# Kernel optimization log

Measured on AMD Instinct MI355X. Metric: run time of the kernel, lower is better.

Reference implementation:

```python
import jax, jax.numpy as jnp
import numpy as np

N_NODES = 50000
N_RAND_EDGES = 800000
K_HEADS = 4
D = 64
EPS = 1e-8


def setup_inputs() -> dict:
    key = jax.random.key(0)
    k1, k2, k3, k4, k5, k6 = jax.random.split(key, 6)
    x = jax.random.normal(k1, (N_NODES, D), dtype=jnp.float32)
    # edge_index without self loops (module removes then re-adds them), then append self loops
    dst = jax.random.randint(k2, (N_RAND_EDGES,), 0, N_NODES)
    off = jax.random.randint(k3, (N_RAND_EDGES,), 1, N_NODES)
    src = (dst + off) % N_NODES  # guaranteed src != dst
    loops = jnp.arange(N_NODES)
    adj = jnp.stack([jnp.concatenate([dst, loops]), jnp.concatenate([src, loops])]).astype(jnp.int64)
    e = jax.random.uniform(k4, (N_NODES, K_HEADS), dtype=jnp.float32)
    stdv = 1.0 / np.sqrt(D)
    weights = jax.random.uniform(k5, (K_HEADS, D, D), minval=-stdv, maxval=stdv, dtype=jnp.float32)
    # xavier_uniform(gain=1.414) on [K, 2D, 1]
    bound = 1.414 * np.sqrt(6.0 / (2 * D + 1))
    a = jax.random.uniform(k6, (K_HEADS, 2 * D, 1), minval=-bound, maxval=bound, dtype=jnp.float32)
    return {"x": x, "adj": adj, "e": e, "weights": weights, "a": a}


def reference(x, adj, e, weights, a):
    N = x.shape[0]
    O = weights.shape[2]
    dst, src = adj[0], adj[1]  # aggregation destination = adj[0], source = adj[1]
    # per-head projection: h[k] = x @ weights[k]  -> [K, N, O]
    h = jnp.einsum('nd,kdo->kno', x, weights)
    # split attention vector: edge_h @ a == <h[dst], a[:O]> + <h[src], a[O:]>
    a_dst = a[:, :O, 0]   # [K, O]
    a_src = a[:, O:, 0]   # [K, O]
    alpha_dst = jnp.einsum('kno,ko->kn', h, a_dst)  # [K, N]
    alpha_src = jnp.einsum('kno,ko->kn', h, a_src)  # [K, N]
    logits = jax.nn.leaky_relu(alpha_dst[:, dst] + alpha_src[:, src], 0.01)  # [K, E]
    # global (per-head) max subtraction, as in the original
    edge_e = jnp.exp(logits - jnp.max(logits, axis=1, keepdims=True))  # [K, E]
    seg = lambda v: jax.ops.segment_sum(v, dst, num_segments=N)
    denom = jax.vmap(seg)(edge_e) + EPS                                 # [K, N]
    num = jax.vmap(seg)(edge_e[:, :, None] * h[:, src])                 # [K, N, O]
    outputs = num / denom[:, :, None]                                   # [K, N, O]
    out = jnp.einsum('nk,kno->no', e, outputs)                          # mixture over K
    return out + x  # residual
```

## Files before the change

### kernel.cpp

```cpp
#include <hip/hip_runtime.h>
#include <hip/hip_bf16.h>

#define KH 4
#define DIM 64
#define EPSV 1e-8f
#define CSTRIDE 16

typedef __attribute__((ext_vector_type(8))) short bf16x8;
typedef __attribute__((ext_vector_type(4))) float f32x4;
typedef __attribute__((ext_vector_type(2))) float f32x2;

__device__ __forceinline__ float lrelu(float s) { return s > 0.0f ? s : 0.01f * s; }
__device__ __forceinline__ float blo(unsigned u) { return __uint_as_float(u << 16); }
__device__ __forceinline__ float bhi(unsigned u) { return __uint_as_float(u & 0xFFFF0000u); }
__device__ __forceinline__ unsigned short f2b(float f) {
    unsigned u = __float_as_uint(f);
    u += 0x7FFFu + ((u >> 16) & 1u);
    return (unsigned short)(u >> 16);
}

__device__ __forceinline__ unsigned char f2e4m3(float f) {
    unsigned u = __float_as_uint(f);
    unsigned sgn = (u >> 31) << 7;
    float af = fabsf(f);
    if (af >= 0.015625f) {
        unsigned mag = u & 0x7FFFFFFFu;
        unsigned biased = mag - (120u << 23);
        unsigned em = biased >> 20;
        unsigned rem = biased & 0xFFFFFu;
        em += (rem > 0x80000u) ? 1u : ((rem == 0x80000u) ? (em & 1u) : 0u);
        if (em > 126u) em = 126u;
        return (unsigned char)(sgn | em);
    } else {
        int m = (int)rintf(af * 512.0f);
        if (m >= 8) return (unsigned char)(sgn | 8u);
        return (unsigned char)(sgn | (unsigned)m);
    }
}

__device__ __forceinline__ unsigned pk_e4m3(float a, float b) {
#if __has_builtin(__builtin_amdgcn_cvt_pk_fp8_f32)
    return (unsigned)__builtin_amdgcn_cvt_pk_fp8_f32(a, b, 0, false) & 0xFFFFu;
#else
    return (unsigned)f2e4m3(a) | ((unsigned)f2e4m3(b) << 8);
#endif
}

__device__ __forceinline__ void e4m3x4_to_f32(unsigned v, float& h0, float& h1,
                                              float& h2, float& h3) {
#if __has_builtin(__builtin_amdgcn_cvt_pk_f32_fp8)
    f32x2 lo = __builtin_amdgcn_cvt_pk_f32_fp8(v, false);
    f32x2 hi = __builtin_amdgcn_cvt_pk_f32_fp8(v, true);
    h0 = lo.x; h1 = lo.y; h2 = hi.x; h3 = hi.y;
#else
    auto dec = [](unsigned b) -> float {
        unsigned s = b >> 7, em = b & 0x7Fu;
        float r;
        if (em >= 8u) r = __uint_as_float((em << 20) + (120u << 23));
        else r = (float)em * 0.001953125f;
        return s ? -r : r;
    };
    h0 = dec(v & 0xFF); h1 = dec((v >> 8) & 0xFF);
    h2 = dec((v >> 16) & 0xFF); h3 = dec(v >> 24);
#endif
}

__global__ void __launch_bounds__(256, 1)
k_prep(const float* __restrict__ W, bf16x8* __restrict__ Wf) {
    int t = threadIdx.x;
    int k = t >> 6;
    int l = t & 63;
    int s = l & 15;
    int q = l >> 4;
    const float* Wk = W + k * DIM * DIM;
#pragma unroll
    for (int tile = 0; tile < 4; ++tile)
#pragma unroll
        for (int c = 0; c < 2; ++c) {
            const float* wp = Wk + (size_t)(32 * c + 8 * q) * DIM + 16 * tile + s;
            bf16x8 v;
#pragma unroll
            for (int j = 0; j < 8; ++j) v[j] = (short)f2b(wp[(size_t)j * DIM]);
            Wf[(k * 8 + tile * 2 + c) * 64 + l] = v;
        }
}

__global__ void __launch_bounds__(256, 4)
k_hidden(const float* __restrict__ x,
         const bf16x8* __restrict__ Wf,
         const float* __restrict__ a,
         unsigned* __restrict__ h8,
         float* __restrict__ adst,
         float* __restrict__ asrc,
         int* __restrict__ cnt, int N) {
    int t = threadIdx.x;
    int gid = blockIdx.x * 256 + t;
    if (gid < N * CSTRIDE) cnt[gid] = 0;
    int k = t >> 6;
    int l = t & 63;
    int s = l & 15;
    int q = l >> 4;
    int n0 = blockIdx.x * 16;

    bf16x8 Bf[4][2];
#pragma unroll
    for (int tile = 0; tile < 4; ++tile)
#pragma unroll
        for (int c = 0; c < 2; ++c)
            Bf[tile][c] = Wf[(k * 8 + tile * 2 + c) * 64 + l];

    float ad[4], as_[4];
#pragma unroll
    for (int tile = 0; tile < 4; ++tile) {
        ad[tile]  = a[k * 2 * DIM + 16 * tile + s];
        as_[tile] = a[k * 2 * DIM + DIM + 16 * tile + s];
    }

    bf16x8 Af[2];
#pragma unroll
    for (int c = 0; c < 2; ++c) {
        const float* xp = x + (size_t)(n0 + s) * DIM + 32 * c + 8 * q;
#pragma unroll
        for (int j = 0; j < 8; ++j) Af[c][j] = (short)f2b(xp[j]);
    }

    f32x4 acc[4];
#pragma unroll
    for (int tile = 0; tile < 4; ++tile) {
        acc[tile] = (f32x4){0.f, 0.f, 0.f, 0.f};
#pragma unroll
        for (int c = 0; c < 2; ++c)
            acc[tile] = __builtin_amdgcn_mfma_f32_16x16x32_bf16(
                Af[c], Bf[tile][c], acc[tile], 0, 0, 0);
    }

#pragma unroll
    for (int r = 0; r < 4; ++r) {
        float vd = 0.f, vs = 0.f;
#pragma unroll
        for (int tile = 0; tile < 4; ++tile) {
            vd = fmaf(acc[tile][r], ad[tile], vd);
            vs = fmaf(acc[tile][r], as_[tile], vs);
        }
#pragma unroll
        for (int off = 1; off < 16; off <<= 1) {
            vd += __shfl_xor(vd, off);
            vs += __shfl_xor(vs, off);
        }
        if (s == 0) {
            int n = n0 + 4 * q + r;
            adst[n * KH + k] = vd;
            asrc[n * KH + k] = vs;
        }
    }

    __shared__ unsigned char hb[16 * DIM * KH];
#pragma unroll
    for (int tile = 0; tile < 4; ++tile) {
        unsigned p01 = pk_e4m3(acc[tile][0], acc[tile][1]);
        unsigned p23 = pk_e4m3(acc[tile][2], acc[tile][3]);
        int o = 16 * tile + s;
        int col = (o ^ (q << 4));
#pragma unroll
        for (int r = 0; r < 4; ++r) {
            unsigned byte = (r < 2) ? ((p01 >> (8 * r)) & 0xFFu)
                                    : ((p23 >> (8 * (r - 2))) & 0xFFu);
            int n = 4 * q + r;
            hb[(n * DIM + col) * KH + k] = (unsigned char)byte;
        }
    }
    __syncthreads();
    const unsigned* hb4 = (const unsigned*)hb;
#pragma unroll
    for (int it = 0; it < 4; ++it) {
        int w = it * 256 + t;
        int wp = w ^ ((((unsigned)w >> 8) & 3u) << 4);
        h8[(size_t)n0 * DIM + w] = hb4[wp];
    }
}

__global__ void k_bin(const int* __restrict__ dst, const int* __restrict__ src,
                      const float4* __restrict__ adst4, const float4* __restrict__ asrc4,
                      int* __restrict__ cnt, uint4* __restrict__ slots,
                      int cap, int E) {
    int tid = blockIdx.x * blockDim.x + threadIdx.x;
    if (tid * 2 >= E) return;
    int2 d = ((const int2*)dst)[tid];
    int2 s = ((const int2*)src)[tid];
    int sl0 = atomicAdd(&cnt[d.x * CSTRIDE], 1);
    int sl1 = atomicAdd(&cnt[d.y * CSTRIDE], 1);
    float4 ad0 = adst4[d.x], as0 = asrc4[s.x];
    float4 ad1 = adst4[d.y], as1 = asrc4[s.y];
#define EMIT(sl, dn, sn, ad, as)                                              \
    if (sl < cap) {                                                           \
        uint4 sv;                                                             \
        sv.x = (unsigned)sn;                                                  \
        sv.y = (unsigned)f2b(__expf(lrelu(ad.x + as.x))) |                    \
               ((unsigned)f2b(__expf(lrelu(ad.y + as.y))) << 16);             \
        sv.z = (unsigned)f2b(__expf(lrelu(ad.z + as.z))) |                    \
               ((unsigned)f2b(__expf(lrelu(ad.w + as.w))) << 16);             \
        sv.w = 0u;                                                            \
        slots[(size_t)dn * cap + sl] = sv;                                    \
    }
    EMIT(sl0, d.x, s.x, ad0, as0)
    EMIT(sl1, d.y, s.y, ad1, as1)
#undef EMIT
}

__global__ void __launch_bounds__(256, 8)
k_aggr(const int* __restrict__ cnt, const uint4* __restrict__ slots,
       const unsigned* __restrict__ h8,
       const float* __restrict__ efeat, const float* __restrict__ x,
       float* __restrict__ out, int cap, int N) {
    int n = __builtin_amdgcn_readfirstlane(blockIdx.x * 4 + (threadIdx.x >> 6));
    if (n >= N) return;
    int o = threadIdx.x & 63;
    int deg = cnt[n * CSTRIDE]; if (deg > cap) deg = cap;
    const uint4* bs = slots + (size_t)n * cap;
    float v0 = 0.f, v1 = 0.f, v2 = 0.f, v3 = 0.f;
    float d0 = 0.f, d1 = 0.f, d2 = 0.f, d3 = 0.f;
#define ACC(sv, hv)                                                           \
    {                                                                         \
        float h0, h1, h2, h3;                                                 \
        e4m3x4_to_f32(hv, h0, h1, h2, h3);                                    \
        float w;                                                              \
        w = blo(sv.y); v0 = fmaf(w, h0, v0); d0 += w;                         \
        w = bhi(sv.y); v1 = fmaf(w, h1, v1); d1 += w;                         \
        w = blo(sv.z); v2 = fmaf(w, h2, v2); d2 += w;                         \
        w = bhi(sv.z); v3 = fmaf(w, h3, v3); d3 += w;                         \
    }
    int i = 0;
    if (deg >= 4) {
        uint4 p0 = bs[0], p1 = bs[1], p2 = bs[2], p3 = bs[3];
        for (; i + 8 <= deg; i += 4) {
            uint4 q0 = bs[i + 4], q1 = bs[i + 5], q2 = bs[i + 6], q3 = bs[i + 7];
            unsigned a0 = h8[(size_t)p0.x * DIM + o];
            unsigned a1 = h8[(size_t)p1.x * DIM + o];
            unsigned a2 = h8[(size_t)p2.x * DIM + o];
            unsigned a3 = h8[(size_t)p3.x * DIM + o];
            ACC(p0, a0) ACC(p1, a1) ACC(p2, a2) ACC(p3, a3)
            p0 = q0; p1 = q1; p2 = q2; p3 = q3;
        }
        unsigned a0 = h8[(size_t)p0.x * DIM + o];
        unsigned a1 = h8[(size_t)p1.x * DIM + o];
        unsigned a2 = h8[(size_t)p2.x * DIM + o];
        unsigned a3 = h8[(size_t)p3.x * DIM + o];
        ACC(p0, a0) ACC(p1, a1) ACC(p2, a2) ACC(p3, a3)
        i += 4;
    }
    for (; i < deg; ++i) {
        uint4 sv = bs[i];
        unsigned hv = h8[(size_t)sv.x * DIM + o];
        ACC(sv, hv)
    }
#undef ACC
    float4 ef = ((const float4*)efeat)[n];
    float c0 = ef.x / (d0 + EPSV), c1 = ef.y / (d1 + EPSV);
    float c2 = ef.z / (d2 + EPSV), c3 = ef.w / (d3 + EPSV);
    size_t oi = (size_t)n * DIM + o;
    out[oi] = x[oi] + c0 * v0 + c1 * v1 + c2 * v2 + c3 * v3;
}

extern "C" void kernel_launch(void* const* d_in, const int* in_sizes, int n_in,
                              void* d_out, int out_size, void* d_ws, size_t ws_size,
                              hipStream_t stream) {
    const float* x = (const float*)d_in[0];
    const int* adj = (const int*)d_in[1];
    const float* efeat = (const float*)d_in[2];
    const float* W = (const float*)d_in[3];
    const float* a = (const float*)d_in[4];
    float* out = (float*)d_out;

    int N = in_sizes[0] / DIM;
    int E = in_sizes[1] / 2;
    const int* dst = adj;
    const int* src = adj + E;
    int nbhid = (N + 15) / 16;

    unsigned* h8 = (unsigned*)d_ws;
    float* adst = (float*)(h8 + (size_t)N * DIM);
    float* asrc = adst + (size_t)N * KH;
    int* cnt = (int*)(asrc + (size_t)N * KH);
    bf16x8* Wf = (bf16x8*)(cnt + (size_t)N * CSTRIDE);
    uint4* slots = (uint4*)(Wf + KH * 8 * 64);
    size_t used = (size_t)((char*)slots - (char*)d_ws);
    int cap = (int)((ws_size - used) / ((size_t)N * 16));
    if (cap > 64) cap = 64;

    k_prep<<<1, 256, 0, stream>>>(W, Wf);

    k_hidden<<<nbhid, 256, 0, stream>>>(x, Wf, a, h8, adst, asrc, cnt, N);

    int npair = E / 2;
    k_bin<<<(npair + 255) / 256, 256, 0, stream>>>(dst, src, (const float4*)adst,
                                                   (const float4*)asrc, cnt,
                                                   slots, cap, E);

    k_aggr<<<(N + 3) / 4, 256, 0, stream>>>(cnt, slots, h8, efeat, x, out, cap, N);
}
```

Baseline: 166.6 us.

## Partition edges into destination-range buckets before scattering to per-node slots

Replaces the single binning kernel with two passes. The first computes edge weights and appends records to 8 buckets keyed by destination range, using wave-aggregated atomics. The second scatters each bucket into per-node slots, so each pass touches a smaller region of cnt and slots and should have better cache locality. The cost is an extra kernel launch, an extra round trip of 16-byte records through global memory, and more workspace for the buckets.

```diff
diff --git a/kernel.cpp b/kernel.cpp
--- a/kernel.cpp
+++ b/kernel.cpp
@@ -66,8 +66,10 @@
 }
 
 __global__ void __launch_bounds__(256, 1)
-k_prep(const float* __restrict__ W, bf16x8* __restrict__ Wf) {
+k_prep(const float* __restrict__ W, bf16x8* __restrict__ Wf,
+       int* __restrict__ bktCnt) {
     int t = threadIdx.x;
+    if (t < 128) bktCnt[t] = 0;
     int k = t >> 6;
     int l = t & 63;
     int s = l & 15;
@@ -179,32 +181,72 @@
     }
 }
 
-__global__ void k_bin(const int* __restrict__ dst, const int* __restrict__ src,
-                      const float4* __restrict__ adst4, const float4* __restrict__ asrc4,
-                      int* __restrict__ cnt, uint4* __restrict__ slots,
-                      int cap, int E) {
-    int tid = blockIdx.x * blockDim.x + threadIdx.x;
-    if (tid * 2 >= E) return;
-    int2 d = ((const int2*)dst)[tid];
-    int2 s = ((const int2*)src)[tid];
-    int sl0 = atomicAdd(&cnt[d.x * CSTRIDE], 1);
-    int sl1 = atomicAdd(&cnt[d.y * CSTRIDE], 1);
-    float4 ad0 = adst4[d.x], as0 = asrc4[s.x];
-    float4 ad1 = adst4[d.y], as1 = asrc4[s.y];
-#define EMIT(sl, dn, sn, ad, as)                                              \
-    if (sl < cap) {                                                           \
-        uint4 sv;                                                             \
-        sv.x = (unsigned)sn;                                                  \
-        sv.y = (unsigned)f2b(__expf(lrelu(ad.x + as.x))) |                    \
-               ((unsigned)f2b(__expf(lrelu(ad.y + as.y))) << 16);             \
-        sv.z = (unsigned)f2b(__expf(lrelu(ad.z + as.z))) |                    \
-               ((unsigned)f2b(__expf(lrelu(ad.w + as.w))) << 16);             \
-        sv.w = 0u;                                                            \
-        slots[(size_t)dn * cap + sl] = sv;                                    \
-    }
-    EMIT(sl0, d.x, s.x, ad0, as0)
-    EMIT(sl1, d.y, s.y, ad1, as1)
-#undef EMIT
+__global__ void __launch_bounds__(256, 8)
+k_part(const int* __restrict__ dst, const int* __restrict__ src,
+       const float4* __restrict__ adst4, const float4* __restrict__ asrc4,
+       int* __restrict__ bktCnt, uint4* __restrict__ bkt,
+       int capB, int psz, int npair) {
+    int lane = threadIdx.x & 63;
+    unsigned long long ltm = (1ull << lane) - 1ull;
+    int stride = gridDim.x * blockDim.x;
+    for (int i = blockIdx.x * blockDim.x + threadIdx.x; i < npair; i += stride) {
+        int2 d = ((const int2*)dst)[i];
+        int2 s = ((const int2*)src)[i];
+        float4 ad0 = adst4[d.x], as0 = asrc4[s.x];
+        float4 ad1 = adst4[d.y], as1 = asrc4[s.y];
+#define PUT(dn, sn, ad, as)                                                   \
+    {                                                                         \
+        uint4 rec;                                                            \
+        rec.x = (unsigned)(dn);                                               \
+        rec.y = (unsigned)f2b(__expf(lrelu(ad.x + as.x))) |                   \
+                ((unsigned)f2b(__expf(lrelu(ad.y + as.y))) << 16);            \
+        rec.z = (unsigned)f2b(__expf(lrelu(ad.z + as.z))) |                   \
+                ((unsigned)f2b(__expf(lrelu(ad.w + as.w))) << 16);            \
+        rec.w = (unsigned)(sn);                                               \
+        unsigned b = (unsigned)(dn) / (unsigned)psz;                          \
+        unsigned long long mask = 0;                                          \
+        for (unsigned bb = 0; bb < 8; ++bb) {                                 \
+            unsigned long long m = __ballot(b == bb);                         \
+            if (b == bb) mask = m;                                            \
+        }                                                                     \
+        int rank = __popcll(mask & ltm);                                      \
+        int leader = __ffsll((long long)mask) - 1;                            \
+        int base = 0;                                                         \
+        if (lane == leader) base = atomicAdd(&bktCnt[b * 16], __popcll(mask));\
+        base = __shfl(base, leader);                                          \
+        int pos = base + rank;                                                \
+        if (pos < capB) bkt[(size_t)b * capB + pos] = rec;                    \
+    }
+        PUT(d.x, s.x, ad0, as0)
+        PUT(d.y, s.y, ad1, as1)
+#undef PUT
+    }
+}
+
+__global__ void __launch_bounds__(256, 8)
+k_scat(const int* __restrict__ bktCnt, const uint4* __restrict__ bkt,
+       int* __restrict__ cnt, uint4* __restrict__ slots,
+       int cap, int capB) {
+    int p  = blockIdx.x & 7;
+    int bp = blockIdx.x >> 3;
+    int nbp = (int)(gridDim.x >> 3);
+    int m = bktCnt[p * 16];
+    if (m > capB) m = capB;
+    const uint4* bb = bkt + (size_t)p * capB;
+    int stride = nbp * 256;
+    for (int j = bp * 256 + (int)threadIdx.x; j < m; j += stride) {
+        uint4 rec = bb[j];
+        int dn = (int)rec.x;
+        int sl = atomicAdd(&cnt[dn * CSTRIDE], 1);
+        if (sl < cap) {
+            uint4 sv;
+            sv.x = rec.w;
+            sv.y = rec.y;
+            sv.z = rec.z;
+            sv.w = 0u;
+            slots[(size_t)dn * cap + sl] = sv;
+        }
+    }
 }
 
 __global__ void __launch_bounds__(256, 8)
@@ -282,19 +324,26 @@
     float* asrc = adst + (size_t)N * KH;
     int* cnt = (int*)(asrc + (size_t)N * KH);
     bf16x8* Wf = (bf16x8*)(cnt + (size_t)N * CSTRIDE);
-    uint4* slots = (uint4*)(Wf + KH * 8 * 64);
+    int* bktCnt = (int*)(Wf + KH * 8 * 64);
+    int capB = E / 8 + 8192;
+    capB = (capB + 3) & ~3;
+    uint4* bkt = (uint4*)(bktCnt + 128);
+    uint4* slots = bkt + (size_t)8 * capB;
     size_t used = (size_t)((char*)slots - (char*)d_ws);
     int cap = (int)((ws_size - used) / ((size_t)N * 16));
     if (cap > 64) cap = 64;
 
-    k_prep<<<1, 256, 0, stream>>>(W, Wf);
+    k_prep<<<1, 256, 0, stream>>>(W, Wf, bktCnt);
 
     k_hidden<<<nbhid, 256, 0, stream>>>(x, Wf, a, h8, adst, asrc, cnt, N);
 
     int npair = E / 2;
-    k_bin<<<(npair + 255) / 256, 256, 0, stream>>>(dst, src, (const float4*)adst,
-                                                   (const float4*)asrc, cnt,
-                                                   slots, cap, E);
+    int psz = (N + 7) / 8;
+    k_part<<<2048, 256, 0, stream>>>(dst, src, (const float4*)adst,
+                                     (const float4*)asrc, bktCnt, bkt,
+                                     capB, psz, npair);
+
+    k_scat<<<2048, 256, 0, stream>>>(bktCnt, bkt, cnt, slots, cap, capB);
 
     k_aggr<<<(N + 3) / 4, 256, 0, stream>>>(cnt, slots, h8, efeat, x, out, cap, N);
 }
```

New measurement: 404.2 us. 2.43x slower.

## Precompute attention projections via W·a and overlap edge binning with projection

Applied to the files above, without the earlier changes.

Folds the attention vector into the weights (va = W·a) so per-node alpha scores come from a cheap x·va dot product in a new k_alpha kernel, which also zeroes the counters. This removes the dependency of edge binning on the MFMA projection. Binning and the hidden projection are then merged into one launch with disjoint block ranges, so the atomic scatter and the matmul can overlap on the GPU. The cost is an extra small kernel and re-reading x. Alpha is now computed in fp32 from x instead of from the bf16 projection, which changes rounding slightly.

```diff
diff --git a/kernel.cpp b/kernel.cpp
--- a/kernel.cpp
+++ b/kernel.cpp
@@ -66,7 +66,8 @@
 }
 
 __global__ void __launch_bounds__(256, 1)
-k_prep(const float* __restrict__ W, bf16x8* __restrict__ Wf) {
+k_prep(const float* __restrict__ W, const float* __restrict__ a,
+       bf16x8* __restrict__ Wf, float* __restrict__ va) {
     int t = threadIdx.x;
     int k = t >> 6;
     int l = t & 63;
@@ -83,114 +84,61 @@
             for (int j = 0; j < 8; ++j) v[j] = (short)f2b(wp[(size_t)j * DIM]);
             Wf[(k * 8 + tile * 2 + c) * 64 + l] = v;
         }
+    int d = l;
+    const float* wr = Wk + (size_t)d * DIM;
+    const float* ak = a + k * 2 * DIM;
+    float sd = 0.f, ss = 0.f;
+#pragma unroll
+    for (int o = 0; o < DIM; ++o) {
+        float w = wr[o];
+        sd = fmaf(w, ak[o], sd);
+        ss = fmaf(w, ak[DIM + o], ss);
+    }
+    va[k * DIM + d] = sd;
+    va[256 + k * DIM + d] = ss;
+}
+
+__global__ void __launch_bounds__(256, 8)
+k_alpha(const float* __restrict__ x, const float* __restrict__ va,
+        float* __restrict__ adst, float* __restrict__ asrc,
+        int* __restrict__ cnt, int N) {
+    int gid = blockIdx.x * 256 + threadIdx.x;
+    if (gid < N * 8) {
+        int z = gid * 2;
+        cnt[z] = 0; cnt[z + 1] = 0;
+    }
+    int n = gid >> 3;
+    if (n >= N) return;
+    int j = gid & 7;
+    const float4* xr = (const float4*)(x + (size_t)n * DIM);
+    const float4* vr = (const float4*)(va + (size_t)j * DIM);
+    float s = 0.f;
+#pragma unroll
+    for (int i = 0; i < 16; ++i) {
+        float4 xv = xr[i], vv = vr[i];
+        s = fmaf(xv.x, vv.x, s); s = fmaf(xv.y, vv.y, s);
+        s = fmaf(xv.z, vv.z, s); s = fmaf(xv.w, vv.w, s);
+    }
+    if (j < 4) adst[n * KH + j] = s;
+    else       asrc[n * KH + (j - 4)] = s;
 }
 
 __global__ void __launch_bounds__(256, 4)
-k_hidden(const float* __restrict__ x,
-         const bf16x8* __restrict__ Wf,
-         const float* __restrict__ a,
-         unsigned* __restrict__ h8,
-         float* __restrict__ adst,
-         float* __restrict__ asrc,
-         int* __restrict__ cnt, int N) {
-    int t = threadIdx.x;
-    int gid = blockIdx.x * 256 + t;
-    if (gid < N * CSTRIDE) cnt[gid] = 0;
-    int k = t >> 6;
-    int l = t & 63;
-    int s = l & 15;
-    int q = l >> 4;
-    int n0 = blockIdx.x * 16;
-
-    bf16x8 Bf[4][2];
-#pragma unroll
-    for (int tile = 0; tile < 4; ++tile)
-#pragma unroll
-        for (int c = 0; c < 2; ++c)
-            Bf[tile][c] = Wf[(k * 8 + tile * 2 + c) * 64 + l];
-
-    float ad[4], as_[4];
-#pragma unroll
-    for (int tile = 0; tile < 4; ++tile) {
-        ad[tile]  = a[k * 2 * DIM + 16 * tile + s];
-        as_[tile] = a[k * 2 * DIM + DIM + 16 * tile + s];
-    }
-
-    bf16x8 Af[2];
-#pragma unroll
-    for (int c = 0; c < 2; ++c) {
-        const float* xp = x + (size_t)(n0 + s) * DIM + 32 * c + 8 * q;
-#pragma unroll
-        for (int j = 0; j < 8; ++j) Af[c][j] = (short)f2b(xp[j]);
-    }
-
-    f32x4 acc[4];
-#pragma unroll
-    for (int tile = 0; tile < 4; ++tile) {
-        acc[tile] = (f32x4){0.f, 0.f, 0.f, 0.f};
-#pragma unroll
-        for (int c = 0; c < 2; ++c)
-            acc[tile] = __builtin_amdgcn_mfma_f32_16x16x32_bf16(
-                Af[c], Bf[tile][c], acc[tile], 0, 0, 0);
-    }
-
-#pragma unroll
-    for (int r = 0; r < 4; ++r) {
-        float vd = 0.f, vs = 0.f;
-#pragma unroll
-        for (int tile = 0; tile < 4; ++tile) {
-            vd = fmaf(acc[tile][r], ad[tile], vd);
-            vs = fmaf(acc[tile][r], as_[tile], vs);
-        }
-#pragma unroll
-        for (int off = 1; off < 16; off <<= 1) {
-            vd += __shfl_xor(vd, off);
-            vs += __shfl_xor(vs, off);
-        }
-        if (s == 0) {
-            int n = n0 + 4 * q + r;
-            adst[n * KH + k] = vd;
-            asrc[n * KH + k] = vs;
-        }
-    }
-
+k_fused(const float* __restrict__ x, const bf16x8* __restrict__ Wf,
+        const int* __restrict__ dst, const int* __restrict__ src,
+        const float4* __restrict__ adst4, const float4* __restrict__ asrc4,
+        int* __restrict__ cnt, uint4* __restrict__ slots,
+        unsigned* __restrict__ h8, int cap, int E, int nbbin) {
     __shared__ unsigned char hb[16 * DIM * KH];
-#pragma unroll
-    for (int tile = 0; tile < 4; ++tile) {
-        unsigned p01 = pk_e4m3(acc[tile][0], acc[tile][1]);
-        unsigned p23 = pk_e4m3(acc[tile][2], acc[tile][3]);
-        int o = 16 * tile + s;
-        int col = (o ^ (q << 4));
-#pragma unroll
-        for (int r = 0; r < 4; ++r) {
-            unsigned byte = (r < 2) ? ((p01 >> (8 * r)) & 0xFFu)
-                                    : ((p23 >> (8 * (r - 2))) & 0xFFu);
-            int n = 4 * q + r;
-            hb[(n * DIM + col) * KH + k] = (unsigned char)byte;
-        }
-    }
-    __syncthreads();
-    const unsigned* hb4 = (const unsigned*)hb;
-#pragma unroll
-    for (int it = 0; it < 4; ++it) {
-        int w = it * 256 + t;
-        int wp = w ^ ((((unsigned)w >> 8) & 3u) << 4);
-        h8[(size_t)n0 * DIM + w] = hb4[wp];
-    }
-}
-
-__global__ void k_bin(const int* __restrict__ dst, const int* __restrict__ src,
-                      const float4* __restrict__ adst4, const float4* __restrict__ asrc4,
-                      int* __restrict__ cnt, uint4* __restrict__ slots,
-                      int cap, int E) {
-    int tid = blockIdx.x * blockDim.x + threadIdx.x;
-    if (tid * 2 >= E) return;
-    int2 d = ((const int2*)dst)[tid];
-    int2 s = ((const int2*)src)[tid];
-    int sl0 = atomicAdd(&cnt[d.x * CSTRIDE], 1);
-    int sl1 = atomicAdd(&cnt[d.y * CSTRIDE], 1);
-    float4 ad0 = adst4[d.x], as0 = asrc4[s.x];
-    float4 ad1 = adst4[d.y], as1 = asrc4[s.y];
+    if ((int)blockIdx.x < nbbin) {
+        int tid = blockIdx.x * 256 + threadIdx.x;
+        if (tid * 2 >= E) return;
+        int2 d = ((const int2*)dst)[tid];
+        int2 s = ((const int2*)src)[tid];
+        int sl0 = atomicAdd(&cnt[d.x * CSTRIDE], 1);
+        int sl1 = atomicAdd(&cnt[d.y * CSTRIDE], 1);
+        float4 ad0 = adst4[d.x], as0 = asrc4[s.x];
+        float4 ad1 = adst4[d.y], as1 = asrc4[s.y];
 #define EMIT(sl, dn, sn, ad, as)                                              \
     if (sl < cap) {                                                           \
         uint4 sv;                                                             \
@@ -202,9 +150,65 @@
         sv.w = 0u;                                                            \
         slots[(size_t)dn * cap + sl] = sv;                                    \
     }
-    EMIT(sl0, d.x, s.x, ad0, as0)
-    EMIT(sl1, d.y, s.y, ad1, as1)
+        EMIT(sl0, d.x, s.x, ad0, as0)
+        EMIT(sl1, d.y, s.y, ad1, as1)
 #undef EMIT
+        return;
+    }
+    int t = threadIdx.x;
+    int k = t >> 6;
+    int l = t & 63;
+    int s = l & 15;
+    int q = l >> 4;
+    int n0 = ((int)blockIdx.x - nbbin) * 16;
+
+    bf16x8 Bf[4][2];
+#pragma unroll
+    for (int tile = 0; tile < 4; ++tile)
+#pragma unroll
+        for (int c = 0; c < 2; ++c)
+            Bf[tile][c] = Wf[(k * 8 + tile * 2 + c) * 64 + l];
+
+    bf16x8 Af[2];
+#pragma unroll
+    for (int c = 0; c < 2; ++c) {
+        const float* xp = x + (size_t)(n0 + s) * DIM + 32 * c + 8 * q;
+#pragma unroll
+        for (int j = 0; j < 8; ++j) Af[c][j] = (short)f2b(xp[j]);
+    }
+
+    f32x4 acc[4];
+#pragma unroll
+    for (int tile = 0; tile < 4; ++tile) {
+        acc[tile] = (f32x4){0.f, 0.f, 0.f, 0.f};
+#pragma unroll
+        for (int c = 0; c < 2; ++c)
+            acc[tile] = __builtin_amdgcn_mfma_f32_16x16x32_bf16(
+                Af[c], Bf[tile][c], acc[tile], 0, 0, 0);
+    }
+
+#pragma unroll
+    for (int tile = 0; tile < 4; ++tile) {
+        unsigned p01 = pk_e4m3(acc[tile][0], acc[tile][1]);
+        unsigned p23 = pk_e4m3(acc[tile][2], acc[tile][3]);
+        int o = 16 * tile + s;
+        int col = (o ^ (q << 4));
+#pragma unroll
+        for (int r = 0; r < 4; ++r) {
+            unsigned byte = (r < 2) ? ((p01 >> (8 * r)) & 0xFFu)
+                                    : ((p23 >> (8 * (r - 2))) & 0xFFu);
+            int n = 4 * q + r;
+            hb[(n * DIM + col) * KH + k] = (unsigned char)byte;
+        }
+    }
+    __syncthreads();
+    const unsigned* hb4 = (const unsigned*)hb;
+#pragma unroll
+    for (int it = 0; it < 4; ++it) {
+        int w = it * 256 + t;
+        int wp = w ^ ((((unsigned)w >> 8) & 3u) << 4);
+        h8[(size_t)n0 * DIM + w] = hb4[wp];
+    }
 }
 
 __global__ void __launch_bounds__(256, 8)
@@ -276,25 +280,28 @@
     const int* dst = adj;
     const int* src = adj + E;
     int nbhid = (N + 15) / 16;
+    int npair = E / 2;
+    int nbbin = (npair + 255) / 256;
 
     unsigned* h8 = (unsigned*)d_ws;
     float* adst = (float*)(h8 + (size_t)N * DIM);
     float* asrc = adst + (size_t)N * KH;
     int* cnt = (int*)(asrc + (size_t)N * KH);
     bf16x8* Wf = (bf16x8*)(cnt + (size_t)N * CSTRIDE);
-    uint4* slots = (uint4*)(Wf + KH * 8 * 64);
+    float* va = (float*)(Wf + KH * 8 * 64);
+    uint4* slots = (uint4*)(va + 512);
     size_t used = (size_t)((char*)slots - (char*)d_ws);
     int cap = (int)((ws_size - used) / ((size_t)N * 16));
     if (cap > 64) cap = 64;
 
-    k_prep<<<1, 256, 0, stream>>>(W, Wf);
-
-    k_hidden<<<nbhid, 256, 0, stream>>>(x, Wf, a, h8, adst, asrc, cnt, N);
-
-    int npair = E / 2;
-    k_bin<<<(npair + 255) / 256, 256, 0, stream>>>(dst, src, (const float4*)adst,
-                                                   (const float4*)asrc, cnt,
-                                                   slots, cap, E);
+    k_prep<<<1, 256, 0, stream>>>(W, a, Wf, va);
+
+    k_alpha<<<(N * 8 + 255) / 256, 256, 0, stream>>>(x, va, adst, asrc, cnt, N);
+
+    k_fused<<<nbbin + nbhid, 256, 0, stream>>>(x, Wf, dst, src,
+                                               (const float4*)adst,
+                                               (const float4*)asrc,
+                                               cnt, slots, h8, cap, E, nbbin);
 
     k_aggr<<<(N + 3) / 4, 256, 0, stream>>>(cnt, slots, h8, efeat, x, out, cap, N);
 }
```

After: 178.2 us. 6.9% more time.
